# Optimization experiments

Hardware: AMD Instinct MI355X
Metric: run time of the kernel (lower is better)

## Reference

```python
import jax, jax.numpy as jnp
import numpy as np
from jax import lax

DIM = 768
SLICES = 12
HEADS = 16
P = 8                      # window_size
CS = DIM // SLICES         # channels per group = 64
HD = DIM // HEADS          # head_dim = 48
BLK = HD // SLICES         # mask block = 4


def group_norm(x, w, b, groups, eps=1e-5):
    # torch GroupNorm: normalize over (C//groups, H, W) per group, biased var
    B, C, H, W = x.shape
    xg = x.reshape(B, groups, (C // groups) * H * W)
    mu = xg.mean(axis=2, keepdims=True)
    var = xg.var(axis=2, keepdims=True)
    xn = ((xg - mu) * lax.rsqrt(var + eps)).reshape(B, C, H, W)
    return xn * w[None, :, None, None] + b[None, :, None, None]


def gconv1x1(x, w, b, groups):
    # grouped 1x1 conv == block-diagonal matmul over channel groups
    B, C, H, W = x.shape
    Co = w.shape[0]
    xg = x.reshape(B, groups, C // groups, H * W)
    wg = w.reshape(groups, Co // groups, C // groups)
    out = jnp.einsum('goi,bgin->bgon', wg, xg).reshape(B, Co, H, W)
    return out + b[None, :, None, None]


def dwconv3(x, w, b):
    # depthwise 3x3, padding 1 (SAME)
    out = lax.conv_general_dilated(x, w, (1, 1), 'SAME',
                                   feature_group_count=x.shape[1],
                                   dimension_numbers=('NCHW', 'OIHW', 'NCHW'))
    return out + b[None, :, None, None]


def gelu(x):
    return jax.nn.gelu(x, approximate=False)  # torch nn.GELU default = exact erf


def tca_forward(y, norm1_w, norm1_b, cpe_w, cpe_b, cpe_nw, cpe_nb,
                qw, qb, kw, kb, vw, vb, pw, pb,
                norm2_w, norm2_b, f1w, f1b, f2w, f2b):
    B, C, H, W = y.shape
    w1, w2 = H // P, W // P
    # window partition: b c (w1 p1) (w2 p2) -> (b w1 w2) c p1 p2
    yw = y.reshape(B, C, w1, P, w2, P).transpose(0, 2, 4, 1, 3, 5).reshape(B * w1 * w2, C, P, P)
    yn = group_norm(yw, norm1_w, norm1_b, SLICES)
    # ConvPosEnc: x + gelu(groupnorm(dwconv(x)))
    feat = group_norm(dwconv3(yn, cpe_w, cpe_b), cpe_nw, cpe_nb, SLICES)
    yn = yn + gelu(feat)
    q = gconv1x1(yn, qw, qb, SLICES)
    k = gconv1x1(yn, kw, kb, SLICES)
    v = gconv1x1(yn, vw, vb, SLICES)
    Bp = yn.shape[0]
    N = P * P
    # torch view(B,N,C//h,h): channel c = d*HEADS + head  ->  (Bp, HD, HEADS, N)
    def split(t):
        return t.reshape(Bp, HD, HEADS, N).transpose(0, 2, 1, 3)  # (Bp, h, hd, N)
    qh, kh, vh = split(q), split(k), split(v)
    scale = HD ** -0.5
    attn = jnp.einsum('bhdn,bhen->bhde', qh * scale, kh)  # channel-attention: (hd x hd)
    idx = jnp.arange(HD)
    mask = (idx[None, :] // BLK) > (idx[:, None] // BLK)  # block-causal over channel slices
    attn = jnp.where(mask[None, None], -jnp.inf, attn)
    attn = jax.nn.softmax(attn, axis=-1)
    out = jnp.einsum('bhde,bhen->bhdn', attn, vh)
    out = out.transpose(0, 2, 1, 3).reshape(Bp, C, P, P)  # back to c = d*HEADS + head
    out = gconv1x1(out, pw, pb, SLICES)
    # window reverse
    out = out.reshape(B, w1, w2, C, P, P).transpose(0, 3, 1, 4, 2, 5).reshape(B, C, H, W)
    tgt = y + out
    t2 = group_norm(tgt, norm2_w, norm2_b, SLICES)
    t2 = gconv1x1(gelu(gconv1x1(t2, f1w, f1b, SLICES)), f2w, f2b, SLICES)
    return tgt + t2


def setup_inputs():
    key = jax.random.key(0)
    ks = jax.random.split(key, 9)
    B, H, W = 2, 256, 256
    f32 = jnp.float32
    d = {}
    d['y'] = jax.random.normal(ks[0], (B, DIM, H, W), f32)
    d['norm1_w'] = jnp.ones((DIM,), f32); d['norm1_b'] = jnp.zeros((DIM,), f32)
    d['cpe_w'] = jax.random.normal(ks[1], (DIM, 1, 3, 3), f32) * 0.1
    d['cpe_b'] = jnp.zeros((DIM,), f32)
    d['cpe_nw'] = jnp.ones((DIM,), f32); d['cpe_nb'] = jnp.zeros((DIM,), f32)
    d['qw'] = jax.random.normal(ks[2], (DIM, CS), f32) * 0.05; d['qb'] = jnp.zeros((DIM,), f32)
    d['kw'] = jax.random.normal(ks[3], (DIM, CS), f32) * 0.05; d['kb'] = jnp.zeros((DIM,), f32)
    d['vw'] = jax.random.normal(ks[4], (DIM, CS), f32) * 0.05; d['vb'] = jnp.zeros((DIM,), f32)
    d['pw'] = jax.random.normal(ks[5], (DIM, CS), f32) * 0.05; d['pb'] = jnp.zeros((DIM,), f32)
    d['norm2_w'] = jnp.ones((DIM,), f32); d['norm2_b'] = jnp.zeros((DIM,), f32)
    d['f1w'] = jax.random.normal(ks[6], (DIM, CS), f32) * 0.05; d['f1b'] = jnp.zeros((DIM,), f32)
    d['f2w'] = jax.random.normal(ks[7], (DIM, CS), f32) * 0.05; d['f2b'] = jnp.zeros((DIM,), f32)
    return d


def reference(y, norm1_w, norm1_b, cpe_w, cpe_b, cpe_nw, cpe_nb,
              qw, qb, kw, kb, vw, vb, pw, pb,
              norm2_w, norm2_b, f1w, f1b, f2w, f2b):
    return tca_forward(y, norm1_w, norm1_b, cpe_w, cpe_b, cpe_nw, cpe_nb,
                       qw, qb, kw, kb, vw, vb, pw, pb,
                       norm2_w, norm2_b, f1w, f1b, f2w, f2b)
```

## Files before the change

kernel.cpp:

```cpp
#include <hip/hip_runtime.h>
#include <hip/hip_bf16.h>

#define IMG 256
#define NPOS 65536

typedef __attribute__((ext_vector_type(8))) short short8;
typedef __attribute__((ext_vector_type(4))) float f32x4;

__device__ __forceinline__ float gelu_exact(float x){
  return 0.5f * x * (1.0f + erff(x * 0.7071067811865475f));
}

__device__ __forceinline__ short f2b(float x){
  __hip_bfloat16 hh = __float2bfloat16(x);
  short s;
  __builtin_memcpy(&s, &hh, sizeof(s));
  return s;
}

__device__ __forceinline__ float b2f(short s){
  unsigned int u = ((unsigned int)(unsigned short)s) << 16;
  float f;
  __builtin_memcpy(&f, &u, sizeof(f));
  return f;
}

template<int NWAVES>
__device__ __forceinline__ void block_reduce2(float& s, float& s2, float* red){
  __syncthreads();
  #pragma unroll
  for (int off=32; off>0; off>>=1){ s += __shfl_down(s, off); s2 += __shfl_down(s2, off); }
  int lane = threadIdx.x & 63, w = threadIdx.x >> 6;
  if (lane==0){ red[w*2]=s; red[w*2+1]=s2; }
  __syncthreads();
  if (threadIdx.x==0){
    float a=0.f, bb=0.f;
    #pragma unroll
    for (int i=0;i<NWAVES;i++){ a+=red[i*2]; bb+=red[i*2+1]; }
    red[2*NWAVES]=a; red[2*NWAVES+1]=bb;
  }
  __syncthreads();
  s=red[2*NWAVES]; s2=red[2*NWAVES+1];
}

__global__ __launch_bounds__(1024) void w_cvt(
    const float* __restrict__ w0, const float* __restrict__ w1,
    const float* __restrict__ w2, const float* __restrict__ w3,
    const float* __restrict__ w4, const float* __restrict__ w5,
    short* __restrict__ outw)
{
  const int mi = blockIdx.y;
  const float* src = mi==0?w0: mi==1?w1: mi==2?w2: mi==3?w3: mi==4?w4: w5;
  const int i = blockIdx.x*1024 + threadIdx.x;
  outw[(size_t)mi*49152 + i] = f2b(src[i]);
}

__global__ __launch_bounds__(256) void k_ab(
    const float* __restrict__ y,
    const float* __restrict__ n1w, const float* __restrict__ n1b,
    const float* __restrict__ cw,  const float* __restrict__ cb,
    const float* __restrict__ cnw, const float* __restrict__ cnb,
    const short* __restrict__ qwB, const float* __restrict__ qb,
    const short* __restrict__ kwB, const float* __restrict__ kb,
    const short* __restrict__ vwB, const float* __restrict__ vb,
    short* __restrict__ qG, short* __restrict__ kG, short* __restrict__ vG,
    int win0)
{
  __shared__ char SMB[32768];
  const int t = threadIdx.x;
  const int w = t>>6, ln = t&63;
  const int bid = blockIdx.x;
  const int nwq = gridDim.x >> 3;
  const int wl  = (bid & 7) * nwq + (bid >> 3);
  const int win = win0 + wl;
  const int b = win>>10, W1=(win>>5)&31, W2=win&31;
  const size_t ybase = (size_t)b*768*(size_t)NPOS + (size_t)(W1*8)*IMG + (W2*8);
  const int g = blockIdx.y*4 + w;
  char* region = SMB + w*8192;

  {
    const int p1 = ln>>3, p2 = ln&7;
    const bool up = p1>0, dn = p1<7, lt = p2>0, rt = p2<7;
    const float* yg = y + ybase + (size_t)(g*64)*NPOS + (size_t)p1*IMG + p2;
    const int swzofs = (ln&7)<<4;
    char* slotbase = region + ln*128;

    float s=0.f, s2=0.f;
    #pragma unroll
    for (int c0=0;c0<64;c0+=8){
      short8 pk;
      #pragma unroll
      for (int j=0;j<8;++j){
        float v = yg[(size_t)(c0+j)*NPOS];
        s += v; s2 += v*v;
        pk[j] = f2b(v);
      }
      *(short8*)(slotbase + ((c0*2) ^ swzofs)) = pk;
    }
    #pragma unroll
    for (int off=32; off>0; off>>=1){ s += __shfl_xor(s, off); s2 += __shfl_xor(s2, off); }
    const float mean = s * (1.f/4096.f);
    const float rstd = rsqrtf(s2*(1.f/4096.f) - mean*mean + 1e-5f);

    float sc=0.f, sc2=0.f;
    #pragma unroll 1
    for (int c0=0;c0<64;c0+=8){
      short8 y8 = *(const short8*)(slotbase + ((c0*2) ^ swzofs));
      #pragma unroll
      for (int j=0;j<8;++j){
        const int cg = g*64 + c0 + j;
        float a = n1w[cg]*rstd;
        float x = fmaf(b2f(y8[j]), a, n1b[cg] - mean*a);
        float nmm = __shfl(x, (ln-9)&63);
        float nm0 = __shfl(x, (ln-8)&63);
        float nmp = __shfl(x, (ln-7)&63);
        float n0m = __shfl(x, (ln-1)&63);
        float n0p = __shfl(x, (ln+1)&63);
        float npm = __shfl(x, (ln+7)&63);
        float np0 = __shfl(x, (ln+8)&63);
        float npp = __shfl(x, (ln+9)&63);
        const float* wp = cw + cg*9;
        float acc = cb[cg];
        acc = fmaf(wp[0], (up&&lt)?nmm:0.f, acc);
        acc = fmaf(wp[1], up?nm0:0.f, acc);
        acc = fmaf(wp[2], (up&&rt)?nmp:0.f, acc);
        acc = fmaf(wp[3], lt?n0m:0.f, acc);
        acc = fmaf(wp[4], x, acc);
        acc = fmaf(wp[5], rt?n0p:0.f, acc);
        acc = fmaf(wp[6], (dn&&lt)?npm:0.f, acc);
        acc = fmaf(wp[7], dn?np0:0.f, acc);
        acc = fmaf(wp[8], (dn&&rt)?npp:0.f, acc);
        sc += acc; sc2 += acc*acc;
      }
    }
    #pragma unroll
    for (int off=32; off>0; off>>=1){ sc += __shfl_xor(sc, off); sc2 += __shfl_xor(sc2, off); }
    const float mean2 = sc * (1.f/4096.f);
    const float rstd2 = rsqrtf(sc2*(1.f/4096.f) - mean2*mean2 + 1e-5f);

    #pragma unroll 1
    for (int c0=0;c0<64;c0+=8){
      short8 y8 = *(const short8*)(slotbase + ((c0*2) ^ swzofs));
      short8 o8;
      #pragma unroll
      for (int j=0;j<8;++j){
        const int cg = g*64 + c0 + j;
        float a = n1w[cg]*rstd;
        float x = fmaf(b2f(y8[j]), a, n1b[cg] - mean*a);
        float nmm = __shfl(x, (ln-9)&63);
        float nm0 = __shfl(x, (ln-8)&63);
        float nmp = __shfl(x, (ln-7)&63);
        float n0m = __shfl(x, (ln-1)&63);
        float n0p = __shfl(x, (ln+1)&63);
        float npm = __shfl(x, (ln+7)&63);
        float np0 = __shfl(x, (ln+8)&63);
        float npp = __shfl(x, (ln+9)&63);
        const float* wp = cw + cg*9;
        float acc = cb[cg];
        acc = fmaf(wp[0], (up&&lt)?nmm:0.f, acc);
        acc = fmaf(wp[1], up?nm0:0.f, acc);
        acc = fmaf(wp[2], (up&&rt)?nmp:0.f, acc);
        acc = fmaf(wp[3], lt?n0m:0.f, acc);
        acc = fmaf(wp[4], x, acc);
        acc = fmaf(wp[5], rt?n0p:0.f, acc);
        acc = fmaf(wp[6], (dn&&lt)?npm:0.f, acc);
        acc = fmaf(wp[7], dn?np0:0.f, acc);
        acc = fmaf(wp[8], (dn&&rt)?npp:0.f, acc);
        float f = (acc - mean2)*rstd2*cnw[cg] + cnb[cg];
        o8[j] = f2b(x + gelu_exact(f));
      }
      *(short8*)(slotbase + ((c0*2) ^ swzofs)) = o8;
    }
  }

  const int l15 = ln&15, c4 = ln>>4, kb8 = c4*8, rbase = c4*4;
  #pragma unroll 1
  for (int mat=0; mat<3; ++mat){
    const short* WB = mat==0?qwB:(mat==1?kwB:vwB);
    const float* Bb = mat==0?qb:(mat==1?kb:vb);
    short* dst = mat==0?qG:(mat==1?kG:vG);
    short8 afr[4][2];
    float bias[4][4];
    #pragma unroll
    for (int mt2=0;mt2<4;++mt2){
      #pragma unroll
      for (int ks=0;ks<2;++ks)
        afr[mt2][ks] = *(const short8*)&WB[(size_t)(g*64+mt2*16+l15)*64 + ks*32 + kb8];
      #pragma unroll
      for (int r=0;r<4;++r)
        bias[mt2][r] = Bb[g*64 + mt2*16 + rbase + r];
    }
    #pragma unroll
    for (int nt=0;nt<4;++nt){
      const int pos = nt*16 + l15;
      short8 b0 = *(const short8*)(region + pos*128 + ((      kb8*2) ^ ((pos&7)<<4)));
      short8 b1 = *(const short8*)(region + pos*128 + ((64 + kb8*2) ^ ((pos&7)<<4)));
      #pragma unroll
      for (int mt2=0;mt2<4;++mt2){
        f32x4 acc = {0.f,0.f,0.f,0.f};
        acc = __builtin_amdgcn_mfma_f32_16x16x32_bf16(afr[mt2][0], b0, acc, 0,0,0);
        acc = __builtin_amdgcn_mfma_f32_16x16x32_bf16(afr[mt2][1], b1, acc, 0,0,0);
        #pragma unroll
        for (int r=0;r<4;++r){
          const int hh = rbase + r;
          float val = acc[r] + bias[mt2][r];
          size_t addr = ((size_t)(wl*16 + hh)*48 + 4*g + mt2)*64 + pos;
          dst[addr] = f2b(mat==0 ? val * 0.14433756729740643f : val);
        }
      }
    }
  }
}

__global__ __launch_bounds__(1024) void k_cp(
    const short* __restrict__ qG, const short* __restrict__ kG,
    const short* __restrict__ vG,
    const float* __restrict__ y,
    const short* __restrict__ pwB, const float* __restrict__ pb,
    float* __restrict__ out, float* __restrict__ part, int win0)
{
  extern __shared__ short SM[];
  const int t = threadIdx.x;
  const int h = t>>6, ln = t&63;
  const int bid = blockIdx.x;
  const int nwq = gridDim.x >> 3;
  const int wl  = (bid & 7) * nwq + (bid >> 3);
  const int win = win0 + wl;
  const int b = win>>10, W1=(win>>5)&31, W2=win&31;
  const size_t ybase = (size_t)b*768*(size_t)NPOS + (size_t)(W1*8)*IMG + (W2*8);
  const int l15 = ln&15, c4 = ln>>4, kb8 = c4*8, rbase = c4*4;
  const size_t hbase = (size_t)(wl*16+h)*48;
  short* R = SM + h*4096;

  short8 kf[3][2], qf[3][2];
  #pragma unroll
  for (int tt=0;tt<3;++tt)
    #pragma unroll
    for (int ks=0;ks<2;++ks){
      kf[tt][ks] = *(const short8*)&kG[(hbase + 16*tt + l15)*64 + ks*32 + kb8];
      qf[tt][ks] = *(const short8*)&qG[(hbase + 16*tt + l15)*64 + ks*32 + kb8];
    }
  f32x4 Su[6];
  const int DTa[6] = {0,1,1,2,2,2};
  const int ETa[6] = {0,0,1,0,1,2};
  #pragma unroll
  for (int u=0;u<6;++u){
    f32x4 acc = {0.f,0.f,0.f,0.f};
    acc = __builtin_amdgcn_mfma_f32_16x16x32_bf16(kf[ETa[u]][0], qf[DTa[u]][0], acc, 0,0,0);
    acc = __builtin_amdgcn_mfma_f32_16x16x32_bf16(kf[ETa[u]][1], qf[DTa[u]][1], acc, 0,0,0);
    Su[u] = acc;
  }

  float inv3[3];
  #pragma unroll
  for (int dt=0;dt<3;++dt){
    const int ub = (dt==0)?0:((dt==1)?1:3);
    float m = -1e30f;
    #pragma unroll
    for (int et=0; et<=dt; ++et)
      #pragma unroll
      for (int r=0;r<4;++r){
        bool valid = (et<dt) || ((rbase + r) <= (l15|3));
        if (valid) m = fmaxf(m, Su[ub+et][r]);
      }
    m = fmaxf(m, __shfl_xor(m,16));
    m = fmaxf(m, __shfl_xor(m,32));
    float sm = 0.f;
    #pragma unroll
    for (int et=0; et<=dt; ++et)
      #pragma unroll
      for (int r=0;r<4;++r){
        bool valid = (et<dt) || ((rbase + r) <= (l15|3));
        float p = valid ? expf(Su[ub+et][r] - m) : 0.f;
        Su[ub+et][r] = p; sm += p;
      }
    sm += __shfl_xor(sm,16);
    sm += __shfl_xor(sm,32);
    inv3[dt] = 1.f/sm;
  }

  short8 z8 = {0,0,0,0,0,0,0,0};
  #pragma unroll
  for (int nblk=0;nblk<8;++nblk){
    short8 v8 = z8;
    if (ln < 48) v8 = *(const short8*)&vG[(hbase + ln)*64 + nblk*8];
    #pragma unroll
    for (int j=0;j<8;++j){
      int n = nblk*8 + j;
      R[n*64 + (((ln>>3) ^ (n&7))<<3) + (ln&7)] = v8[j];
    }
  }
  short8 bv[4][2];
  #pragma unroll
  for (int nt=0;nt<4;++nt){
    const int n = 16*nt + l15;
    bv[nt][0] = *(const short8*)&R[n*64 + ((c4 ^ (n&7))<<3)];
    bv[nt][1] = *(const short8*)&R[n*64 + (((4+c4) ^ (n&7))<<3)];
  }

  #pragma unroll
  for (int i_=0;i_<6;++i_) *(short8*)&R[i_*512 + ln*8] = z8;
  #pragma unroll
  for (int dt=0;dt<3;++dt){
    const int ub = (dt==0)?0:((dt==1)?1:3);
    const int d = 16*dt + l15;
    #pragma unroll
    for (int et=0; et<=dt; ++et)
      #pragma unroll
      for (int r=0;r<4;++r){
        int e = 16*et + rbase + r;
        R[d*64 + (((e>>3) ^ (d&7))<<3) + (e&7)] = f2b(Su[ub+et][r]*inv3[dt]);
      }
  }
  short8 aP[4];
  const int PDT[4] = {0,1,2,2}, PKS[4] = {0,0,0,1};
  #pragma unroll
  for (int i_=0;i_<4;++i_){
    int d = 16*PDT[i_] + l15;
    int ch = PKS[i_]*4 + c4;
    aP[i_] = *(const short8*)&R[d*64 + ((ch ^ (d&7))<<3)];
  }

  __syncthreads();

  #pragma unroll
  for (int nt=0;nt<4;++nt){
    const int n = 16*nt + l15;
    f32x4 O0 = {0.f,0.f,0.f,0.f};
    f32x4 O1 = {0.f,0.f,0.f,0.f};
    f32x4 O2 = {0.f,0.f,0.f,0.f};
    O0 = __builtin_amdgcn_mfma_f32_16x16x32_bf16(aP[0], bv[nt][0], O0, 0,0,0);
    O1 = __builtin_amdgcn_mfma_f32_16x16x32_bf16(aP[1], bv[nt][0], O1, 0,0,0);
    O2 = __builtin_amdgcn_mfma_f32_16x16x32_bf16(aP[2], bv[nt][0], O2, 0,0,0);
    O2 = __builtin_amdgcn_mfma_f32_16x16x32_bf16(aP[3], bv[nt][1], O2, 0,0,0);
    #pragma unroll
    for (int r=0;r<4;++r){
      const int swz = (((2*r + (h>>3)) ^ (n&7))<<3) + (h&7);
      SM[(c4     )*4096 + n*64 + swz] = f2b(O0[r]);
      SM[(4 + c4 )*4096 + n*64 + swz] = f2b(O1[r]);
      SM[(8 + c4 )*4096 + n*64 + swz] = f2b(O2[r]);
    }
  }

  __syncthreads();

  #pragma unroll 1
  for (int j=0;j<3;++j){
    const int u = h*3 + j;
    const int g = u>>2, mt = u&3;
    short8 aw[2];
    float bi[4];
    #pragma unroll
    for (int ks=0;ks<2;++ks)
      aw[ks] = *(const short8*)&pwB[(size_t)(g*64 + mt*16 + l15)*64 + ks*32 + kb8];
    #pragma unroll
    for (int r=0;r<4;++r) bi[r] = pb[g*64 + mt*16 + rbase + r];

    f32x4 acc[4] = {};
    #pragma unroll
    for (int nt=0;nt<4;++nt){
      const int n = 16*nt + l15;
      short8 b0 = *(const short8*)&SM[g*4096 + n*64 + ((c4 ^ (n&7))<<3)];
      short8 b1 = *(const short8*)&SM[g*4096 + n*64 + (((4+c4) ^ (n&7))<<3)];
      acc[nt] = __builtin_amdgcn_mfma_f32_16x16x32_bf16(aw[0], b0, acc[nt], 0,0,0);
      acc[nt] = __builtin_amdgcn_mfma_f32_16x16x32_bf16(aw[1], b1, acc[nt], 0,0,0);
    }
    float s=0.f, s2=0.f;
    #pragma unroll
    for (int nt=0;nt<4;++nt){
      const int n = 16*nt + l15;
      const size_t rowoff = ybase + (size_t)(n>>3)*IMG + (n&7);
      #pragma unroll
      for (int r=0;r<4;++r){
        int m = mt*16 + rbase + r;
        size_t ad = rowoff + (size_t)(g*64+m)*NPOS;
        float o = y[ad] + bi[r] + acc[nt][r];
        out[ad] = o;
        s += o; s2 += o*o;
      }
    }
    #pragma unroll
    for (int off=32; off>0; off>>=1){ s += __shfl_xor(s, off); s2 += __shfl_xor(s2, off); }
    if (ln==0){
      size_t idx = ((size_t)(b*12+g)*1024 + (win&1023))*4 + mt;
      part[idx*2+0]=s; part[idx*2+1]=s2;
    }
  }
}

__global__ __launch_bounds__(256) void k3_stats(
    const float* __restrict__ part, float* __restrict__ stats)
{
  const int bg = blockIdx.x;
  const int t = threadIdx.x;
  float s=0.f, s2=0.f;
  #pragma unroll
  for (int j=0;j<16;++j){
    size_t idx = (size_t)bg*4096 + t*16 + j;
    s  += part[idx*2+0];
    s2 += part[idx*2+1];
  }
  __shared__ float red[10];
  block_reduce2<4>(s,s2,red);
  if (t==0){
    const float Ninv = 1.f/(64.f*65536.f);
    float mean = s*Ninv;
    float var  = s2*Ninv - mean*mean;
    stats[bg*2+0] = mean;
    stats[bg*2+1] = rsqrtf(var + 1e-5f);
  }
}

__global__ __launch_bounds__(256) void k_d(
    const float* __restrict__ n2w, const float* __restrict__ n2b,
    const short* __restrict__ f1wB, const float* __restrict__ f1b,
    const short* __restrict__ f2wB, const float* __restrict__ f2bi,
    const float* __restrict__ stats, float* __restrict__ io)
{
  __shared__ short Xb[4096];
  __shared__ short Hb[4096];
  const int t = threadIdx.x;
  const int pt = blockIdx.x, g = blockIdx.y, b = blockIdx.z;
  const int bg = b*12 + g;
  const float mean = stats[bg*2+0], rstd = stats[bg*2+1];
  const size_t base = ((size_t)(b*768 + g*64))*NPOS + (size_t)pt*64;

  const int wv = t>>6, ln = t&63;
  const int l15 = ln&15, kb8 = (ln>>4)*8, rbase = (ln>>4)*4, c4 = ln>>4;
  const int n = wv*16 + l15;

  float res[16];
  #pragma unroll
  for (int mt=0;mt<4;++mt)
    #pragma unroll
    for (int r=0;r<4;++r)
      res[mt*4+r] = io[base + (size_t)(mt*16 + rbase + r)*NPOS + n];

  {
    const int pp = t>>3, posq = t&7;
    const int ch0 = pp*2;
    const float* p0 = io + base + (size_t)ch0*NPOS + posq*8;
    float4 x00 = *(const float4*)p0;
    float4 x01 = *(const float4*)(p0+4);
    const float* p1 = p0 + NPOS;
    float4 x10 = *(const float4*)p1;
    float4 x11 = *(const float4*)(p1+4);
    float A0 = rstd*n2w[g*64+ch0],   C0 = n2b[g*64+ch0]   - mean*A0;
    float A1 = rstd*n2w[g*64+ch0+1], C1 = n2b[g*64+ch0+1] - mean*A1;
    float va[8] = {x00.x,x00.y,x00.z,x00.w,x01.x,x01.y,x01.z,x01.w};
    float vb[8] = {x10.x,x10.y,x10.z,x10.w,x11.x,x11.y,x11.z,x11.w};
    #pragma unroll
    for (int j=0;j<8;++j){
      int pos = posq*8 + j;
      unsigned int u0 = (unsigned short)f2b(va[j]*A0 + C0);
      unsigned int u1 = (unsigned short)f2b(vb[j]*A1 + C1);
      *(unsigned int*)&Xb[pos*64 + (((ch0>>3) ^ (pos&7))<<3) + (ch0&7)] = u0 | (u1<<16);
    }
  }
  __syncthreads();

  short8 af[4][2];
  #pragma unroll
  for (int mt=0;mt<4;++mt)
    #pragma unroll
    for (int ks=0;ks<2;++ks)
      af[mt][ks] = *(const short8*)&f1wB[(size_t)(g*64 + mt*16 + l15)*64 + ks*32 + kb8];
  f32x4 h[4] = {};
  #pragma unroll
  for (int ks=0;ks<2;++ks){
    short8 bfr = *(const short8*)&Xb[n*64 + (((ks*4 + c4) ^ (n&7))<<3)];
    #pragma unroll
    for (int mt=0;mt<4;++mt)
      h[mt] = __builtin_amdgcn_mfma_f32_16x16x32_bf16(af[mt][ks], bfr, h[mt], 0,0,0);
  }
  #pragma unroll
  for (int mt=0;mt<4;++mt){
    #pragma unroll
    for (int rp=0;rp<4;rp+=2){
      int m = mt*16 + rbase + rp;
      float h0 = gelu_exact(h[mt][rp]   + f1b[g*64+m]);
      float h1 = gelu_exact(h[mt][rp+1] + f1b[g*64+m+1]);
      unsigned int u0 = (unsigned short)f2b(h0);
      unsigned int u1 = (unsigned short)f2b(h1);
      *(unsigned int*)&Hb[n*64 + (((m>>3) ^ (n&7))<<3) + (m&7)] = u0 | (u1<<16);
    }
  }
  __syncthreads();

  #pragma unroll
  for (int mt=0;mt<4;++mt)
    #pragma unroll
    for (int ks=0;ks<2;++ks)
      af[mt][ks] = *(const short8*)&f2wB[(size_t)(g*64 + mt*16 + l15)*64 + ks*32 + kb8];
  f32x4 o[4] = {};
  #pragma unroll
  for (int ks=0;ks<2;++ks){
    short8 bfr = *(const short8*)&Hb[n*64 + (((ks*4 + c4) ^ (n&7))<<3)];
    #pragma unroll
    for (int mt=0;mt<4;++mt)
      o[mt] = __builtin_amdgcn_mfma_f32_16x16x32_bf16(af[mt][ks], bfr, o[mt], 0,0,0);
  }
  #pragma unroll
  for (int mt=0;mt<4;++mt)
    #pragma unroll
    for (int r=0;r<4;++r){
      int m = mt*16 + rbase + r;
      io[base + (size_t)m*NPOS + n] = res[mt*4+r] + o[mt][r] + f2bi[g*64+m];
    }
}

extern "C" void kernel_launch(void* const* d_in, const int* in_sizes, int n_in,
                              void* d_out, int out_size, void* d_ws, size_t ws_size,
                              hipStream_t stream){
  const float* y    = (const float*)d_in[0];
  const float* n1w  = (const float*)d_in[1];
  const float* n1b  = (const float*)d_in[2];
  const float* cw   = (const float*)d_in[3];
  const float* cb   = (const float*)d_in[4];
  const float* cnw  = (const float*)d_in[5];
  const float* cnb  = (const float*)d_in[6];
  const float* qw   = (const float*)d_in[7];
  const float* qb   = (const float*)d_in[8];
  const float* kw   = (const float*)d_in[9];
  const float* kb   = (const float*)d_in[10];
  const float* vw   = (const float*)d_in[11];
  const float* vb   = (const float*)d_in[12];
  const float* pw   = (const float*)d_in[13];
  const float* pb   = (const float*)d_in[14];
  const float* n2w  = (const float*)d_in[15];
  const float* n2b  = (const float*)d_in[16];
  const float* f1w  = (const float*)d_in[17];
  const float* f1b  = (const float*)d_in[18];
  const float* f2w  = (const float*)d_in[19];
  const float* f2b_ = (const float*)d_in[20];
  float* out   = (float*)d_out;

  unsigned char* wsb = (unsigned char*)d_ws;
  float* part  = (float*)wsb;
  float* stats = part + 24*1024*4*2;
  short* wbf   = (short*)(wsb + 786624);
  short* qwB  = wbf;
  short* kwB  = wbf + 49152;
  short* vwB  = wbf + 2*49152;
  short* pwB  = wbf + 3*49152;
  short* f1wB = wbf + 4*49152;
  short* f2wB = wbf + 5*49152;

  int C = 32;
  {
    const int cand[4] = {4,8,16,32};
    for (int i=0;i<4;++i){
      int nw = 2048 / cand[i];
      size_t Y = (size_t)nw * 16 * 48 * 64 * 2;
      if ((size_t)(1<<21) + 3*Y <= ws_size){ C = cand[i]; break; }
    }
  }
  const int nw = 2048 / C;
  const size_t Y = (size_t)nw * 16 * 48 * 64 * 2;
  short* qG  = (short*)(wsb + (1<<21));
  short* kG  = (short*)(wsb + (1<<21) + Y);
  short* vG  = (short*)(wsb + (1<<21) + 2*Y);

  hipLaunchKernelGGL(w_cvt, dim3(48, 6), dim3(1024), 0, stream,
                     qw, kw, vw, pw, f1w, f2w, wbf);

  for (int c=0; c<C; ++c){
    int win0 = c * nw;
    hipLaunchKernelGGL(k_ab, dim3(nw, 3), dim3(256), 0, stream,
                       y, n1w,n1b, cw,cb, cnw,cnb,
                       qwB,qb, kwB,kb, vwB,vb,
                       qG, kG, vG, win0);
    hipLaunchKernelGGL(k_cp, dim3(nw), dim3(1024), 131072, stream,
                       qG, kG, vG, y, pwB, pb, out, part, win0);
  }
  hipLaunchKernelGGL(k3_stats, dim3(24), dim3(256), 0, stream, part, stats);
  hipLaunchKernelGGL(k_d, dim3(1024, 12, 2), dim3(256), 0, stream,
                     n2w,n2b, f1wB,f1b, f2wB,f2b_, stats, out);
}
```

Measured before the change: 1.315 ms.

## Make MLP kernel wave-local to drop block barriers in k_d

Restructures the fused norm2+MLP kernel so each wavefront owns a private 2KB LDS region holding only its own 16 positions. The normalized input and GELU output are written and read within the same wave, which removes both __syncthreads barriers. Each lane now loads the normalized input with scalar per-channel loads instead of the earlier float4 cooperative loads, so global coalescing changes. Relying on wave-synchronous LDS ordering without explicit barriers is a correctness risk if the compiler or hardware reorders accesses.

```diff
diff --git a/kernel.cpp b/kernel.cpp
--- a/kernel.cpp
+++ b/kernel.cpp
@@ -417,8 +417,7 @@
     const short* __restrict__ f2wB, const float* __restrict__ f2bi,
     const float* __restrict__ stats, float* __restrict__ io)
 {
-  __shared__ short Xb[4096];
-  __shared__ short Hb[4096];
+  __shared__ char SMB[8192];
   const int t = threadIdx.x;
   const int pt = blockIdx.x, g = blockIdx.y, b = blockIdx.z;
   const int bg = b*12 + g;
@@ -426,87 +425,74 @@
   const size_t base = ((size_t)(b*768 + g*64))*NPOS + (size_t)pt*64;
 
   const int wv = t>>6, ln = t&63;
-  const int l15 = ln&15, kb8 = (ln>>4)*8, rbase = (ln>>4)*4, c4 = ln>>4;
-  const int n = wv*16 + l15;
+  const int l15 = ln&15, c4 = ln>>4, kb8 = c4*8, rbase = c4*4;
+  const int pos = wv*16 + l15;
+  char* region = SMB + wv*2048;
+  const int swz = (l15&7)<<4;
+  char* row = region + l15*128;
 
   float res[16];
   #pragma unroll
   for (int mt=0;mt<4;++mt)
     #pragma unroll
     for (int r=0;r<4;++r)
-      res[mt*4+r] = io[base + (size_t)(mt*16 + rbase + r)*NPOS + n];
-
-  {
-    const int pp = t>>3, posq = t&7;
-    const int ch0 = pp*2;
-    const float* p0 = io + base + (size_t)ch0*NPOS + posq*8;
-    float4 x00 = *(const float4*)p0;
-    float4 x01 = *(const float4*)(p0+4);
-    const float* p1 = p0 + NPOS;
-    float4 x10 = *(const float4*)p1;
-    float4 x11 = *(const float4*)(p1+4);
-    float A0 = rstd*n2w[g*64+ch0],   C0 = n2b[g*64+ch0]   - mean*A0;
-    float A1 = rstd*n2w[g*64+ch0+1], C1 = n2b[g*64+ch0+1] - mean*A1;
-    float va[8] = {x00.x,x00.y,x00.z,x00.w,x01.x,x01.y,x01.z,x01.w};
-    float vb[8] = {x10.x,x10.y,x10.z,x10.w,x11.x,x11.y,x11.z,x11.w};
-    #pragma unroll
-    for (int j=0;j<8;++j){
-      int pos = posq*8 + j;
-      unsigned int u0 = (unsigned short)f2b(va[j]*A0 + C0);
-      unsigned int u1 = (unsigned short)f2b(vb[j]*A1 + C1);
-      *(unsigned int*)&Xb[pos*64 + (((ch0>>3) ^ (pos&7))<<3) + (ch0&7)] = u0 | (u1<<16);
-    }
-  }
-  __syncthreads();
-
-  short8 af[4][2];
-  #pragma unroll
-  for (int mt=0;mt<4;++mt)
-    #pragma unroll
-    for (int ks=0;ks<2;++ks)
-      af[mt][ks] = *(const short8*)&f1wB[(size_t)(g*64 + mt*16 + l15)*64 + ks*32 + kb8];
-  f32x4 h[4] = {};
-  #pragma unroll
-  for (int ks=0;ks<2;++ks){
-    short8 bfr = *(const short8*)&Xb[n*64 + (((ks*4 + c4) ^ (n&7))<<3)];
-    #pragma unroll
-    for (int mt=0;mt<4;++mt)
-      h[mt] = __builtin_amdgcn_mfma_f32_16x16x32_bf16(af[mt][ks], bfr, h[mt], 0,0,0);
-  }
+      res[mt*4+r] = io[base + (size_t)(mt*16 + rbase + r)*NPOS + pos];
+
+  #pragma unroll
+  for (int blk=0;blk<2;++blk){
+    short8 pk;
+    #pragma unroll
+    for (int jj=0;jj<8;++jj){
+      const int ch = c4*16 + blk*8 + jj;
+      float v = io[base + (size_t)ch*NPOS + pos];
+      float A = rstd*n2w[g*64+ch];
+      pk[jj] = f2b(fmaf(v, A, n2b[g*64+ch] - mean*A));
+    }
+    *(short8*)(row + ((c4*32 + blk*16) ^ swz)) = pk;
+  }
+
+  short8 xb0 = *(const short8*)(row + ((      kb8*2) ^ swz));
+  short8 xb1 = *(const short8*)(row + ((64 + kb8*2) ^ swz));
+
+  f32x4 hacc[4];
   #pragma unroll
   for (int mt=0;mt<4;++mt){
-    #pragma unroll
-    for (int rp=0;rp<4;rp+=2){
-      int m = mt*16 + rbase + rp;
-      float h0 = gelu_exact(h[mt][rp]   + f1b[g*64+m]);
-      float h1 = gelu_exact(h[mt][rp+1] + f1b[g*64+m+1]);
-      unsigned int u0 = (unsigned short)f2b(h0);
-      unsigned int u1 = (unsigned short)f2b(h1);
-      *(unsigned int*)&Hb[n*64 + (((m>>3) ^ (n&7))<<3) + (m&7)] = u0 | (u1<<16);
-    }
-  }
-  __syncthreads();
-
-  #pragma unroll
-  for (int mt=0;mt<4;++mt)
-    #pragma unroll
-    for (int ks=0;ks<2;++ks)
-      af[mt][ks] = *(const short8*)&f2wB[(size_t)(g*64 + mt*16 + l15)*64 + ks*32 + kb8];
-  f32x4 o[4] = {};
-  #pragma unroll
-  for (int ks=0;ks<2;++ks){
-    short8 bfr = *(const short8*)&Hb[n*64 + (((ks*4 + c4) ^ (n&7))<<3)];
-    #pragma unroll
-    for (int mt=0;mt<4;++mt)
-      o[mt] = __builtin_amdgcn_mfma_f32_16x16x32_bf16(af[mt][ks], bfr, o[mt], 0,0,0);
-  }
-  #pragma unroll
-  for (int mt=0;mt<4;++mt)
+    short8 a0 = *(const short8*)&f1wB[(size_t)(g*64+mt*16+l15)*64 + kb8];
+    short8 a1 = *(const short8*)&f1wB[(size_t)(g*64+mt*16+l15)*64 + 32 + kb8];
+    f32x4 acc = {0.f,0.f,0.f,0.f};
+    acc = __builtin_amdgcn_mfma_f32_16x16x32_bf16(a0, xb0, acc, 0,0,0);
+    acc = __builtin_amdgcn_mfma_f32_16x16x32_bf16(a1, xb1, acc, 0,0,0);
+    hacc[mt] = acc;
+  }
+
+  #pragma unroll
+  for (int mt=0;mt<4;++mt){
+    const int m0 = mt*16 + rbase;
+    float g0 = gelu_exact(hacc[mt][0] + f1b[g*64+m0+0]);
+    float g1 = gelu_exact(hacc[mt][1] + f1b[g*64+m0+1]);
+    float g2 = gelu_exact(hacc[mt][2] + f1b[g*64+m0+2]);
+    float g3 = gelu_exact(hacc[mt][3] + f1b[g*64+m0+3]);
+    unsigned int u0 = (unsigned int)(unsigned short)f2b(g0) | ((unsigned int)(unsigned short)f2b(g1)<<16);
+    unsigned int u1 = (unsigned int)(unsigned short)f2b(g2) | ((unsigned int)(unsigned short)f2b(g3)<<16);
+    *(uint2*)(row + ((mt*32 + c4*8) ^ swz)) = make_uint2(u0, u1);
+  }
+
+  short8 hb0 = *(const short8*)(row + ((      kb8*2) ^ swz));
+  short8 hb1 = *(const short8*)(row + ((64 + kb8*2) ^ swz));
+
+  #pragma unroll
+  for (int mt=0;mt<4;++mt){
+    short8 a0 = *(const short8*)&f2wB[(size_t)(g*64+mt*16+l15)*64 + kb8];
+    short8 a1 = *(const short8*)&f2wB[(size_t)(g*64+mt*16+l15)*64 + 32 + kb8];
+    f32x4 acc = {0.f,0.f,0.f,0.f};
+    acc = __builtin_amdgcn_mfma_f32_16x16x32_bf16(a0, hb0, acc, 0,0,0);
+    acc = __builtin_amdgcn_mfma_f32_16x16x32_bf16(a1, hb1, acc, 0,0,0);
     #pragma unroll
     for (int r=0;r<4;++r){
-      int m = mt*16 + rbase + r;
-      io[base + (size_t)m*NPOS + n] = res[mt*4+r] + o[mt][r] + f2bi[g*64+m];
-    }
+      const int m = mt*16 + rbase + r;
+      io[base + (size_t)m*NPOS + pos] = res[mt*4+r] + acc[r] + f2bi[g*64+m];
+    }
+  }
 }
 
 extern "C" void kernel_launch(void* const* d_in, const int* in_sizes, int n_in,
```

Result: slower. 1.351 ms (+2.8%).
